# Performance work log

Measured on AMD Instinct MI355X. Metric: run time of the kernel, lower is better.

Reference implementation:

```python
import jax, jax.numpy as jnp
import numpy as np

T, K, N = 4096, 4096, 11008
EPS = 1e-5


def setup_inputs() -> dict:
    key = jax.random.key(0)
    k1, k2, k3, k4 = jax.random.split(key, 4)
    input_tensor = jax.random.normal(k1, (1, T, K), dtype=jnp.bfloat16)
    # int8 weights in [-127, 127]
    weight = jax.random.randint(k2, (N, K), -127, 128, dtype=jnp.int8)
    # per-output-channel weight scale, small positive values
    weight_scale = (jax.random.uniform(k3, (N, 1), dtype=jnp.float32) * 0.02 + 1e-4)
    bias = jax.random.normal(k4, (N,), dtype=jnp.bfloat16)
    return {"input_tensor": input_tensor, "weight": weight,
            "weight_scale": weight_scale, "bias": bias}


def _quantize_per_token_absmax(x):
    # x: [T, K] float -> int8 quant [T, K], float32 scale [T, 1]
    xf = x.astype(jnp.float32)
    absmax = jnp.max(jnp.abs(xf), axis=-1, keepdims=True)  # [T, 1]
    scale = jnp.maximum(absmax, EPS) / 127.0
    q = jnp.clip(jnp.round(xf / scale), -127, 127).astype(jnp.int8)
    return q, scale


def reference(input_tensor, weight, weight_scale, bias):
    x = jnp.squeeze(input_tensor, axis=0)                  # [T, K]
    x_q, x_scale = _quantize_per_token_absmax(x)           # int8 [T,K], f32 [T,1]
    # int8 GEMM with int32 accumulation: [T, K] @ [K, N]
    acc = jax.lax.dot_general(
        x_q, weight.T,
        dimension_numbers=(((1,), (0,)), ((), ())),
        preferred_element_type=jnp.int32,
    )
    # dequantize: per-token scale * per-channel scale
    out = (acc.astype(jnp.float32) * x_scale * weight_scale.T).astype(jnp.bfloat16)
    out = out + bias
    return out[None, :, :]                                  # [1, T, N]
```

## Files before the change

### kernel.cpp

```cpp
#include <hip/hip_runtime.h>
#include <hip/hip_bf16.h>
#include <stdint.h>

#define T_DIM 4096
#define K_DIM 4096
#define N_DIM 11008

#define XQ_OFF 0
#define XS_OFF 16777216
#define W8_OFF 16793600

typedef __attribute__((ext_vector_type(4))) int v4i;

__global__ __launch_bounds__(256) void prep_kernel(
    const float* __restrict__ x, int8_t* __restrict__ xq, float* __restrict__ xs,
    const int* __restrict__ w32, int8_t* __restrict__ w8)
{
    if (blockIdx.x < T_DIM / 4) {
        const int wid   = threadIdx.x >> 6;
        const int lane  = threadIdx.x & 63;
        const int token = blockIdx.x * 4 + wid;

        const float* xrow = x + (size_t)token * K_DIM;

        float4 v[16];
        float am = 0.0f;
#pragma unroll
        for (int j = 0; j < 16; ++j) {
            v[j] = *(const float4*)(xrow + (size_t)(j * 64 + lane) * 4);
            am = fmaxf(am, fmaxf(fmaxf(fabsf(v[j].x), fabsf(v[j].y)),
                                 fmaxf(fabsf(v[j].z), fabsf(v[j].w))));
        }
#pragma unroll
        for (int m = 1; m < 64; m <<= 1)
            am = fmaxf(am, __shfl_xor(am, m, 64));

        const float scale = fmaxf(am, 1e-5f) / 127.0f;
        if (lane == 0) xs[token] = scale;

        uint32_t* qrow = (uint32_t*)(xq + (size_t)token * K_DIM);
#pragma unroll
        for (int j = 0; j < 16; ++j) {
            int q0 = min(127, max(-127, (int)rintf(v[j].x / scale)));
            int q1 = min(127, max(-127, (int)rintf(v[j].y / scale)));
            int q2 = min(127, max(-127, (int)rintf(v[j].z / scale)));
            int q3 = min(127, max(-127, (int)rintf(v[j].w / scale)));
            qrow[j * 64 + lane] = ((uint32_t)(uint8_t)(int8_t)q0)       |
                                  ((uint32_t)(uint8_t)(int8_t)q1 << 8)  |
                                  ((uint32_t)(uint8_t)(int8_t)q2 << 16) |
                                  ((uint32_t)(uint8_t)(int8_t)q3 << 24);
        }
    } else {
        const size_t tid = (size_t)(blockIdx.x - T_DIM / 4) * 256 + threadIdx.x;
        const int4* src = (const int4*)w32 + tid * 4;
        uint32_t o[4];
#pragma unroll
        for (int i = 0; i < 4; ++i) {
            int4 a = src[i];
            o[i] = ((uint32_t)a.x & 0xFFu) | (((uint32_t)a.y & 0xFFu) << 8) |
                   (((uint32_t)a.z & 0xFFu) << 16) | ((uint32_t)a.w << 24);
        }
        *(uint4*)(w8 + tid * 16) = make_uint4(o[0], o[1], o[2], o[3]);
    }
}

#define BM 256
#define BN 256
#define BKB 64
#define NT (K_DIM / BKB)
#define BUF_SZ 16384

__global__ __launch_bounds__(512, 2) void gemm_i8_kernel(
    const int8_t* __restrict__ xq, const int8_t* __restrict__ w8,
    const float* __restrict__ xs, const float* __restrict__ wsc,
    const __hip_bfloat16* __restrict__ bias, float* __restrict__ out)
{
    __shared__ int8_t lds[4 * 2 * BUF_SZ];

    constexpr int NBN = N_DIM / BN;
    constexpr int NWG = (T_DIM / BM) * NBN;
    constexpr int CPX = NWG / 8;

    const int bid = blockIdx.x;
    const int b2  = (bid % 8) * CPX + bid / 8;
    const int bm  = b2 / NBN;
    const int bn  = b2 % NBN;

    const int tid  = threadIdx.x;
    const int wid  = tid >> 6;
    const int lane = tid & 63;
    const int wm   = wid >> 2;
    const int wn   = wid & 3;

    const int fr = lane & 15, kg = lane >> 4;
    int offA[8], offB[4];
#pragma unroll
    for (int mi = 0; mi < 8; ++mi) {
        const int row = wm * 128 + mi * 16 + fr;
        offA[mi] = row * 64 + ((kg ^ ((row >> 1) & 3)) << 4);
    }
#pragma unroll
    for (int ni = 0; ni < 4; ++ni) {
        const int row = wn * 64 + ni * 16 + fr;
        offB[ni] = row * 64 + ((kg ^ ((row >> 1) & 3)) << 4);
    }

    const int srow  = tid >> 2;
    const int sslot = tid & 3;
    const int r0 = srow, r1 = 128 + srow;
    const int c0 = sslot ^ ((r0 >> 1) & 3);
    const int c1 = sslot ^ ((r1 >> 1) & 3);
    const int8_t* gA0 = xq + (size_t)(bm * BM + r0) * K_DIM + c0 * 16;
    const int8_t* gA1 = xq + (size_t)(bm * BM + r1) * K_DIM + c1 * 16;
    const int8_t* gB0 = w8 + (size_t)(bn * BM + r0) * K_DIM + c0 * 16;
    const int8_t* gB1 = w8 + (size_t)(bn * BM + r1) * K_DIM + c1 * 16;
    const int ldsW = wid * 1024;

    v4i acc[8][4];
#pragma unroll
    for (int mi = 0; mi < 8; ++mi)
#pragma unroll
        for (int ni = 0; ni < 4; ++ni) acc[mi][ni] = (v4i){0, 0, 0, 0};

#define STAGE(bufb, mat, Rr, kt)                                                \
    __builtin_amdgcn_global_load_lds(                                           \
        (const __attribute__((address_space(1))) void*)(                        \
            ((mat) ? ((Rr) ? gB1 : gB0) : ((Rr) ? gA1 : gA0)) +                 \
            (size_t)(kt) * BKB),                                                \
        (__attribute__((address_space(3))) void*)(                              \
            lds + ((bufb) * 2 + (mat)) * BUF_SZ + (Rr) * 8192 + ldsW),          \
        16, 0, 0)

#define STAGE_TILE(bufb, kt)                                                    \
    do {                                                                        \
        STAGE(bufb, 0, 0, kt); STAGE(bufb, 0, 1, kt);                           \
        STAGE(bufb, 1, 0, kt); STAGE(bufb, 1, 1, kt);                           \
    } while (0)

    STAGE_TILE(0, 0);
    STAGE_TILE(1, 1);
    STAGE_TILE(2, 2);
    asm volatile("s_waitcnt vmcnt(8)" ::: "memory");
    __builtin_amdgcn_s_barrier();
    asm volatile("" ::: "memory");

    for (int t = 0; t < NT; ++t) {
        const int b  = t & 3;
        const int pb = (t + 3) & 3;
        const int8_t* bA = lds + (b * 2 + 0) * BUF_SZ;
        const int8_t* bB = lds + (b * 2 + 1) * BUF_SZ;

        if (t + 3 < NT) STAGE_TILE(pb, t + 3);

        v4i bF[4], aF[8];
#pragma unroll
        for (int ni = 0; ni < 4; ++ni) bF[ni] = *(const v4i*)(bB + offB[ni]);
#pragma unroll
        for (int mi = 0; mi < 8; ++mi) aF[mi] = *(const v4i*)(bA + offA[mi]);

        __builtin_amdgcn_s_setprio(1);
#pragma unroll
        for (int mi = 0; mi < 8; ++mi)
#pragma unroll
            for (int ni = 0; ni < 4; ++ni)
                acc[mi][ni] = __builtin_amdgcn_mfma_i32_16x16x64_i8(
                    aF[mi], bF[ni], acc[mi][ni], 0, 0, 0);
        __builtin_amdgcn_s_setprio(0);

        if (t < NT - 3)      asm volatile("s_waitcnt vmcnt(8)" ::: "memory");
        else if (t == NT - 3) asm volatile("s_waitcnt vmcnt(4)" ::: "memory");
        else                 asm volatile("s_waitcnt vmcnt(0)" ::: "memory");
        __builtin_amdgcn_s_barrier();
        asm volatile("" ::: "memory");
    }

    const int row0 = bm * BM + wm * 128 + (lane >> 4) * 4;
    const int col0 = bn * BN + wn * 64 + (lane & 15);
#pragma unroll
    for (int mi = 0; mi < 8; ++mi) {
#pragma unroll
        for (int j = 0; j < 4; ++j) {
            const int row = row0 + mi * 16 + j;
            const float xscale = xs[row];
#pragma unroll
            for (int ni = 0; ni < 4; ++ni) {
                const int col = col0 + ni * 16;
                float p_  = (float)acc[mi][ni][j] * xscale * wsc[col];
                float pb_ = __bfloat162float(__float2bfloat16(p_));
                float vb  = __bfloat162float(__float2bfloat16(
                                pb_ + __bfloat162float(bias[col])));
                out[(size_t)row * N_DIM + col] = vb;
            }
        }
    }
#undef STAGE
#undef STAGE_TILE
}

extern "C" void kernel_launch(void* const* d_in, const int* in_sizes, int n_in,
                              void* d_out, int out_size, void* d_ws, size_t ws_size,
                              hipStream_t stream)
{
    const float*          x    = (const float*)d_in[0];
    const int*            w32  = (const int*)d_in[1];
    const float*          wsc  = (const float*)d_in[2];
    const __hip_bfloat16* bias = (const __hip_bfloat16*)d_in[3];
    float*                out  = (float*)d_out;

    int8_t* xq = (int8_t*)d_ws + XQ_OFF;
    float*  xs = (float*)((char*)d_ws + XS_OFF);
    int8_t* w8 = (int8_t*)d_ws + W8_OFF;

    prep_kernel<<<T_DIM / 4 + (N_DIM * (K_DIM / 16)) / 256, 256, 0, stream>>>(
        x, xq, xs, w32, w8);
    gemm_i8_kernel<<<(T_DIM / BM) * (N_DIM / BN), 512, 0, stream>>>(
        xq, w8, xs, wsc, bias, out);
}
```

Before: 265.5 us.

## Double K tile to 128 with two-stage LDS buffering and 8-way swizzle

Raises the K step per LDS tile from 64 to 128 bytes and drops from a 4-deep ring of buffers to double buffering. Each iteration now runs two k-substeps of MFMAs, the XOR swizzle is widened to 8 slots, and global-to-LDS staging is remapped to 8 threads per row. The goal is to halve the number of barrier and waitcnt rounds per K. The cost is only one tile of prefetch in flight, and a full vmcnt(0) drain every iteration may expose memory latency.

```diff
diff --git a/kernel.cpp b/kernel.cpp
--- a/kernel.cpp
+++ b/kernel.cpp
@@ -66,16 +66,16 @@
 
 #define BM 256
 #define BN 256
-#define BKB 64
+#define BKB 128
 #define NT (K_DIM / BKB)
-#define BUF_SZ 16384
+#define MAT_SZ 32768
 
 __global__ __launch_bounds__(512, 2) void gemm_i8_kernel(
     const int8_t* __restrict__ xq, const int8_t* __restrict__ w8,
     const float* __restrict__ xs, const float* __restrict__ wsc,
     const __hip_bfloat16* __restrict__ bias, float* __restrict__ out)
 {
-    __shared__ int8_t lds[4 * 2 * BUF_SZ];
+    __shared__ int8_t lds[2 * 2 * MAT_SZ];
 
     constexpr int NBN = N_DIM / BN;
     constexpr int NWG = (T_DIM / BM) * NBN;
@@ -93,28 +93,30 @@
     const int wn   = wid & 3;
 
     const int fr = lane & 15, kg = lane >> 4;
-    int offA[8], offB[4];
+    int offA[8][2], offB[4][2];
 #pragma unroll
     for (int mi = 0; mi < 8; ++mi) {
         const int row = wm * 128 + mi * 16 + fr;
-        offA[mi] = row * 64 + ((kg ^ ((row >> 1) & 3)) << 4);
+#pragma unroll
+        for (int ks = 0; ks < 2; ++ks)
+            offA[mi][ks] = row * 128 + (((ks * 4 + kg) ^ (row & 7)) << 4);
     }
 #pragma unroll
     for (int ni = 0; ni < 4; ++ni) {
         const int row = wn * 64 + ni * 16 + fr;
-        offB[ni] = row * 64 + ((kg ^ ((row >> 1) & 3)) << 4);
-    }
-
-    const int srow  = tid >> 2;
-    const int sslot = tid & 3;
-    const int r0 = srow, r1 = 128 + srow;
-    const int c0 = sslot ^ ((r0 >> 1) & 3);
-    const int c1 = sslot ^ ((r1 >> 1) & 3);
-    const int8_t* gA0 = xq + (size_t)(bm * BM + r0) * K_DIM + c0 * 16;
-    const int8_t* gA1 = xq + (size_t)(bm * BM + r1) * K_DIM + c1 * 16;
-    const int8_t* gB0 = w8 + (size_t)(bn * BM + r0) * K_DIM + c0 * 16;
-    const int8_t* gB1 = w8 + (size_t)(bn * BM + r1) * K_DIM + c1 * 16;
-    const int ldsW = wid * 1024;
+#pragma unroll
+        for (int ks = 0; ks < 2; ++ks)
+            offB[ni][ks] = row * 128 + (((ks * 4 + kg) ^ (row & 7)) << 4);
+    }
+
+    const int srow  = tid >> 3;
+    const int sslot = tid & 7;
+    const int csw   = (sslot ^ (srow & 7)) * 16;
+    const int8_t* gA = xq + (size_t)(bm * BM + srow) * K_DIM + csw;
+    const int8_t* gB = w8 + (size_t)(bn * BN + srow) * K_DIM + csw;
+    const int ldsT = (tid & 511) * 16 - (lane * 16);
+    const int ldsBase = (tid >> 6) * 1024;
+    (void)ldsT;
 
     v4i acc[8][4];
 #pragma unroll
@@ -122,54 +124,56 @@
 #pragma unroll
         for (int ni = 0; ni < 4; ++ni) acc[mi][ni] = (v4i){0, 0, 0, 0};
 
-#define STAGE(bufb, mat, Rr, kt)                                                \
+#define STAGE(bufb, mat, r, kt)                                                 \
     __builtin_amdgcn_global_load_lds(                                           \
         (const __attribute__((address_space(1))) void*)(                        \
-            ((mat) ? ((Rr) ? gB1 : gB0) : ((Rr) ? gA1 : gA0)) +                 \
-            (size_t)(kt) * BKB),                                                \
+            ((mat) ? gB : gA) + (size_t)(r) * 64 * K_DIM + (size_t)(kt) * BKB), \
         (__attribute__((address_space(3))) void*)(                              \
-            lds + ((bufb) * 2 + (mat)) * BUF_SZ + (Rr) * 8192 + ldsW),          \
+            lds + ((bufb) * 2 + (mat)) * MAT_SZ + (r) * 8192 + ldsBase),        \
         16, 0, 0)
 
 #define STAGE_TILE(bufb, kt)                                                    \
     do {                                                                        \
         STAGE(bufb, 0, 0, kt); STAGE(bufb, 0, 1, kt);                           \
+        STAGE(bufb, 0, 2, kt); STAGE(bufb, 0, 3, kt);                           \
         STAGE(bufb, 1, 0, kt); STAGE(bufb, 1, 1, kt);                           \
+        STAGE(bufb, 1, 2, kt); STAGE(bufb, 1, 3, kt);                           \
     } while (0)
 
     STAGE_TILE(0, 0);
-    STAGE_TILE(1, 1);
-    STAGE_TILE(2, 2);
-    asm volatile("s_waitcnt vmcnt(8)" ::: "memory");
+    asm volatile("s_waitcnt vmcnt(0)" ::: "memory");
     __builtin_amdgcn_s_barrier();
     asm volatile("" ::: "memory");
 
     for (int t = 0; t < NT; ++t) {
-        const int b  = t & 3;
-        const int pb = (t + 3) & 3;
-        const int8_t* bA = lds + (b * 2 + 0) * BUF_SZ;
-        const int8_t* bB = lds + (b * 2 + 1) * BUF_SZ;
-
-        if (t + 3 < NT) STAGE_TILE(pb, t + 3);
-
-        v4i bF[4], aF[8];
-#pragma unroll
-        for (int ni = 0; ni < 4; ++ni) bF[ni] = *(const v4i*)(bB + offB[ni]);
-#pragma unroll
-        for (int mi = 0; mi < 8; ++mi) aF[mi] = *(const v4i*)(bA + offA[mi]);
-
-        __builtin_amdgcn_s_setprio(1);
-#pragma unroll
-        for (int mi = 0; mi < 8; ++mi)
+        const int b  = t & 1;
+        const int pn = b ^ 1;
+        const int8_t* bA = lds + (b * 2 + 0) * MAT_SZ;
+        const int8_t* bB = lds + (b * 2 + 1) * MAT_SZ;
+
+        if (t + 1 < NT) STAGE_TILE(pn, t + 1);
+
+#pragma unroll
+        for (int ks = 0; ks < 2; ++ks) {
+            v4i bF[4], aF[8];
 #pragma unroll
             for (int ni = 0; ni < 4; ++ni)
-                acc[mi][ni] = __builtin_amdgcn_mfma_i32_16x16x64_i8(
-                    aF[mi], bF[ni], acc[mi][ni], 0, 0, 0);
-        __builtin_amdgcn_s_setprio(0);
-
-        if (t < NT - 3)      asm volatile("s_waitcnt vmcnt(8)" ::: "memory");
-        else if (t == NT - 3) asm volatile("s_waitcnt vmcnt(4)" ::: "memory");
-        else                 asm volatile("s_waitcnt vmcnt(0)" ::: "memory");
+                bF[ni] = *(const v4i*)(bB + offB[ni][ks]);
+#pragma unroll
+            for (int mi = 0; mi < 8; ++mi)
+                aF[mi] = *(const v4i*)(bA + offA[mi][ks]);
+
+            __builtin_amdgcn_s_setprio(1);
+#pragma unroll
+            for (int mi = 0; mi < 8; ++mi)
+#pragma unroll
+                for (int ni = 0; ni < 4; ++ni)
+                    acc[mi][ni] = __builtin_amdgcn_mfma_i32_16x16x64_i8(
+                        aF[mi], bF[ni], acc[mi][ni], 0, 0, 0);
+            __builtin_amdgcn_s_setprio(0);
+        }
+
+        asm volatile("s_waitcnt vmcnt(0)" ::: "memory");
         __builtin_amdgcn_s_barrier();
         asm volatile("" ::: "memory");
     }
```

New measurement: 258.0 us. -2.8%, faster.
